# Performance work log

Hardware: AMD Instinct MI355X
Metric: run time of the kernel (lower is better)

## Reference

```python
import jax, jax.numpy as jnp
import numpy as np

INPUT_SIZE = 608
STRIDE = 32
NUM_CLASSES = 20
NMS_THRESH = 0.5
NUM_ANCHOR = 5
ANCHORS = np.array([[1.19, 1.98], [2.79, 4.59], [4.53, 8.92], [8.06, 5.29], [10.32, 10.65]], dtype=np.float32)


def _conv(x, w, b, pad):
    # x: NCHW, w: OIHW
    y = jax.lax.conv_general_dilated(x, w, (1, 1), [(pad, pad), (pad, pad)],
                                     dimension_numbers=('NCHW', 'OIHW', 'NCHW'))
    return y + b[None, :, None, None]


def _leaky(x):
    return jnp.where(x > 0, x, 0.1 * x)


def _reorg(x, s=2):
    # space-to-depth, darknet reorg: [B,C,H,W] -> [B,C*s*s,H/s,W/s]
    B, C, H, W = x.shape
    x = x.reshape(B, C, H // s, s, W // s, s)
    x = x.transpose(0, 3, 5, 1, 2, 4)
    return x.reshape(B, C * s * s, H // s, W // s)


def _forward_boxes_scores(feat_layer2, feat_layer3, w1a, b1a, w1b, b1b, wr, br, w2, b2, wp, bp):
    p5 = _leaky(_conv(feat_layer3, w1a, b1a, 1))
    p5 = _leaky(_conv(p5, w1b, b1b, 1))
    p4 = _reorg(_leaky(_conv(feat_layer2, wr, br, 0)))         # [1,256,19,19]
    p5 = jnp.concatenate([p4, p5], axis=1)                      # [1,1280,19,19]
    p5 = _leaky(_conv(p5, w2, b2, 1))
    pred = _conv(p5, wp, bp, 0)                                 # [1,125,19,19]
    B, C, H, W = pred.shape
    pred = pred.transpose(0, 2, 3, 1).reshape(B, H * W, C)
    conf = pred[:, :, :NUM_ANCHOR].reshape(B, H * W * NUM_ANCHOR, 1)
    cls = pred[:, :, NUM_ANCHOR:(1 + NUM_CLASSES) * NUM_ANCHOR].reshape(B, H * W * NUM_ANCHOR, NUM_CLASSES)
    reg = pred[:, :, (1 + NUM_CLASSES) * NUM_ANCHOR:].reshape(B, H * W, NUM_ANCHOR, 4)
    # decode_xywh
    gy, gx = jnp.meshgrid(jnp.arange(H), jnp.arange(W), indexing='ij')
    grid = jnp.stack([gx, gy], axis=-1).astype(pred.dtype).reshape(1, H * W, 1, 2)
    anchor_wh = jnp.asarray(ANCHORS).reshape(1, 1, NUM_ANCHOR, 2)
    xy = jax.nn.sigmoid(reg[..., :2]) + grid
    wh = jnp.exp(reg[..., 2:]) * anchor_wh
    xywh = jnp.concatenate([xy, wh], axis=-1).reshape(B, -1, 4) * STRIDE
    boxes = jnp.concatenate([xywh[..., :2] - 0.5 * xywh[..., 2:],
                             xywh[..., :2] + 0.5 * xywh[..., 2:]], axis=-1)
    boxes = jnp.clip(boxes[0] / INPUT_SIZE, 0.0, 1.0)           # [N,4]
    scores = jax.nn.sigmoid(conf[0]) * jax.nn.softmax(cls[0], axis=-1)  # [N,20]
    return boxes, scores


def _per_class_nms(boxes, scores, class_mask):
    # greedy sequential NMS, faithful to the torch while-loop (suppress iff IoU > thresh)
    N = boxes.shape[0]
    s = jnp.where(class_mask, scores, -jnp.inf)
    order = jnp.argsort(-s)
    b = boxes[order]
    valid = class_mask[order]
    x1, y1, x2, y2 = b[:, 0], b[:, 1], b[:, 2], b[:, 3]
    areas = (x2 - x1) * (y2 - y1)
    iw = jnp.maximum(1e-10, jnp.minimum(x2[:, None], x2[None, :]) - jnp.maximum(x1[:, None], x1[None, :]))
    ih = jnp.maximum(1e-10, jnp.minimum(y2[:, None], y2[None, :]) - jnp.maximum(y1[:, None], y1[None, :]))
    inter = iw * ih
    iou = inter / (areas[:, None] + areas[None, :] - inter)
    upper = jnp.arange(N)[None, :] > jnp.arange(N)[:, None]
    sup_mat = (iou > NMS_THRESH) & upper

    def body(i, state):
        suppressed, keep = state
        cur = valid[i] & jnp.logical_not(suppressed[i])
        keep = keep.at[i].set(cur)
        suppressed = suppressed | (cur & sup_mat[i])
        return suppressed, keep

    _, keep_sorted = jax.lax.fori_loop(0, N, body, (jnp.zeros(N, bool), jnp.zeros(N, bool)))
    return jnp.zeros(N, bool).at[order].set(keep_sorted)


def setup_inputs() -> dict:
    key = jax.random.key(0)
    ks = jax.random.split(key, 8)
    w = lambda k, shape: jax.random.normal(k, shape, jnp.float32) * 0.01
    return {
        'feat_layer2': jax.random.normal(ks[0], (1, 512, 38, 38), jnp.float32),
        'feat_layer3': jax.random.normal(ks[1], (1, 1024, 19, 19), jnp.float32),
        'w1a': w(ks[2], (1024, 1024, 3, 3)), 'b1a': jnp.zeros((1024,), jnp.float32),
        'w1b': w(ks[3], (1024, 1024, 3, 3)), 'b1b': jnp.zeros((1024,), jnp.float32),
        'wr': w(ks[4], (64, 512, 1, 1)), 'br': jnp.zeros((64,), jnp.float32),
        'w2': w(ks[5], (1024, 1280, 3, 3)), 'b2': jnp.zeros((1024,), jnp.float32),
        'wp': w(ks[6], (125, 1024, 1, 1)), 'bp': jnp.zeros((125,), jnp.float32),
    }


def reference(feat_layer2, feat_layer3, w1a, b1a, w1b, b1b, wr, br, w2, b2, wp, bp):
    boxes, scores_full = _forward_boxes_scores(feat_layer2, feat_layer3,
                                               w1a, b1a, w1b, b1b, wr, br, w2, b2, wp, bp)
    cls_inds = jnp.argmax(scores_full, axis=1)                          # [N]
    scores = jnp.take_along_axis(scores_full, cls_inds[:, None], axis=1)[:, 0]
    masks = cls_inds[None, :] == jnp.arange(NUM_CLASSES)[:, None]       # [20,N]
    keeps = jax.vmap(lambda m: _per_class_nms(boxes, scores, m))(masks)
    keep = jnp.any(keeps, axis=0)                                       # [N] bool, fixed-shape mask
    return boxes, scores, cls_inds, keep
```

## Files before the change

### kernel.cpp

```cpp
#include <hip/hip_runtime.h>

typedef _Float16 f16;
typedef _Float16 f16x8 __attribute__((ext_vector_type(8)));
typedef float f32x4 __attribute__((ext_vector_type(4)));

#define N_BOX 1805
#define NPIX 361
#define NCLS 20
#define GNW 29
#define MB_ROWS 226

__device__ __forceinline__ float leakyf(float x){ return x > 0.f ? x : 0.1f*x; }
__device__ __forceinline__ float sigmoidf_(float x){ return 1.f/(1.f + expf(-x)); }

__global__ void transpose_k(const float* __restrict__ src, float* __restrict__ dst, int R, int C){
  int i = blockIdx.x*256 + threadIdx.x;
  if (i < R*C){ int r = i / C, c = i % C; dst[c*R + r] = src[i]; }
}

__global__ void wprep_packed_k(const float* __restrict__ w, f16* __restrict__ wpk,
                               int Cin, int cpt, int NK){
  int gid = blockIdx.x*256 + threadIdx.x;
  if (gid >= 8*NK*1024) return;
  int g    = gid & 1023;
  int tile = gid >> 10;
  int kc   = tile % NK;
  int cob  = tile / NK;
  int row  = g >> 3, sraw = g & 7;
  int sdata = sraw ^ (row & 7);
  int h = sdata >> 2, jci = sdata & 3;
  int t = kc / cpt;
  int ci0 = (kc - t*cpt)*32 + jci*8;
  int co = cob*128 + row;
  const float* src = w + ((size_t)co*Cin + ci0)*9 + t;
  f16x8 outv;
  #pragma unroll
  for (int k = 0; k < 8; ++k){
    float v = src[(size_t)k*9] * 64.f;
    f16 hi = (f16)v;
    outv[k] = h ? (f16)(v - (float)hi) : hi;
  }
  *(f16x8*)(wpk + (size_t)tile*8192 + g*8) = outv;
}

__global__ void act1prep_k(const float* __restrict__ feat3, f16* __restrict__ ah, f16* __restrict__ al){
  int i = blockIdx.x*256 + threadIdx.x;
  if (i >= NPIX*1024) return;
  int p = i >> 10, c = i & 1023;
  float v = feat3[c*NPIX + p];
  f16 hi = (f16)v; f16 lo = (f16)(v - (float)hi);
  ah[i] = hi; al[i] = lo;
}

__global__ __launch_bounds__(256) void reorg_conv_k(const float* __restrict__ feat2,
    const float* __restrict__ wrT, const float* __restrict__ br,
    f16* __restrict__ cath, f16* __restrict__ catl){
  int c  = threadIdx.x & 63;
  int pq = threadIdx.x >> 6;
  int pix = blockIdx.x*4 + pq;
  int y = pix / 38, x = pix % 38;
  __shared__ float s_in[64][4];
  float acc = br[c];
  for (int cb = 0; cb < 512; cb += 64){
    __syncthreads();
    { int k = threadIdx.x >> 2, pp = threadIdx.x & 3;
      s_in[k][pp] = feat2[(cb + k)*1444 + blockIdx.x*4 + pp]; }
    __syncthreads();
    #pragma unroll
    for (int k = 0; k < 64; ++k)
      acc = fmaf(wrT[(cb+k)*64 + c], s_in[k][pq], acc);
  }
  float v = leakyf(acc);
  int co = ((y & 1)*2 + (x & 1))*64 + c;
  int p = (y>>1)*19 + (x>>1);
  f16 hi = (f16)v; f16 lo = (f16)(v - (float)hi);
  size_t o = (size_t)p*1280 + co;
  cath[o] = hi; catl[o] = lo;
}

__global__ __launch_bounds__(256) void conv_mfma_k(
    const f16* __restrict__ wpk,
    const f16* __restrict__ ahi, const f16* __restrict__ alo,
    float* __restrict__ part, int Cin, int chunks, int cpt, int NK)
{
  int cob = blockIdx.x;
  int px0 = blockIdx.y * 128;
  int ks  = blockIdx.z;
  int kc0 = ks * chunks;
  int tid = threadIdx.x;

  __shared__ f16 sA[2][128*64];
  __shared__ f16 sB[2][128*64];

  const f16* wbase = wpk + ((size_t)cob*NK + kc0)*8192;
  int aost[4];
  #pragma unroll
  for (int j = 0; j < 4; ++j) aost[j] = (tid + j*256)*8;

  int r = tid >> 1, h = tid & 1;
  int wboff[4];
  #pragma unroll
  for (int j = 0; j < 4; ++j)
    wboff[j] = (r*128 + (h*4 + j)*16) ^ ((r & 7) << 4);
  int p = px0 + r;
  int py = p / 19, px = p - py*19;
  const f16* bbase = (h ? alo : ahi);

  int lane = tid & 63, wid = tid >> 6;
  int lrow = lane & 15, lgrp = lane >> 4;
  int wr = wid >> 1, wc = wid & 1;
  int aoffH[4], aoffL[4], boffH[4], boffL[4];
  #pragma unroll
  for (int m = 0; m < 4; ++m){
    int rA = wr*64 + m*16 + lrow;
    aoffH[m] = (rA*128 + lgrp*16)     ^ ((rA & 7) << 4);
    aoffL[m] = (rA*128 + (4+lgrp)*16) ^ ((rA & 7) << 4);
    int rB = wc*64 + m*16 + lrow;
    boffH[m] = (rB*128 + lgrp*16)     ^ ((rB & 7) << 4);
    boffL[m] = (rB*128 + (4+lgrp)*16) ^ ((rB & 7) << 4);
  }

  f32x4 acc[4][4] = {};
  f16x8 sa0, sa1, sa2, sa3, sb0, sb1, sb2, sb3;

  auto LOADK = [&](int i){
    const f16* as = wbase + (size_t)i*8192;
    sa0 = *(const f16x8*)(as + aost[0]);
    sa1 = *(const f16x8*)(as + aost[1]);
    sa2 = *(const f16x8*)(as + aost[2]);
    sa3 = *(const f16x8*)(as + aost[3]);
    int kc = kc0 + i;
    int t = kc / cpt;
    int ci0 = (kc - t*cpt) * 32;
    int dy = t/3, dx = t - dy*3;
    int yy = py + dy - 1, xx = px + dx - 1;
    bool bvalid = (p < NPIX) && ((unsigned)yy < 19u) && ((unsigned)xx < 19u);
    f16x8 z = {};
    sb0 = z; sb1 = z; sb2 = z; sb3 = z;
    if (bvalid){
      const f16* bs = bbase + (size_t)(yy*19+xx)*Cin + ci0;
      sb0 = *(const f16x8*)(bs);
      sb1 = *(const f16x8*)(bs + 8);
      sb2 = *(const f16x8*)(bs + 16);
      sb3 = *(const f16x8*)(bs + 24);
    }
  };
  auto WRITEK = [&](int buf){
    *(f16x8*)(&sA[buf][aost[0]]) = sa0;
    *(f16x8*)(&sA[buf][aost[1]]) = sa1;
    *(f16x8*)(&sA[buf][aost[2]]) = sa2;
    *(f16x8*)(&sA[buf][aost[3]]) = sa3;
    *(f16x8*)((char*)sB[buf] + wboff[0]) = sb0;
    *(f16x8*)((char*)sB[buf] + wboff[1]) = sb1;
    *(f16x8*)((char*)sB[buf] + wboff[2]) = sb2;
    *(f16x8*)((char*)sB[buf] + wboff[3]) = sb3;
  };

  LOADK(0);
  WRITEK(0);
  __syncthreads();

  for (int i = 0; i < chunks; ++i){
    int cur = i & 1;
    bool more = (i + 1 < chunks);
    if (more) LOADK(i + 1);

    f16x8 bh[4], bl[4];
    #pragma unroll
    for (int n = 0; n < 4; ++n){
      bh[n] = *(const f16x8*)((char*)sB[cur] + boffH[n]);
      bl[n] = *(const f16x8*)((char*)sB[cur] + boffL[n]);
    }
    #pragma unroll
    for (int m = 0; m < 4; ++m){
      f16x8 ah = *(const f16x8*)((char*)sA[cur] + aoffH[m]);
      f16x8 al = *(const f16x8*)((char*)sA[cur] + aoffL[m]);
      #pragma unroll
      for (int n = 0; n < 4; ++n){
        acc[m][n] = __builtin_amdgcn_mfma_f32_16x16x32_f16(ah, bh[n], acc[m][n], 0,0,0);
        acc[m][n] = __builtin_amdgcn_mfma_f32_16x16x32_f16(ah, bl[n], acc[m][n], 0,0,0);
        acc[m][n] = __builtin_amdgcn_mfma_f32_16x16x32_f16(al, bh[n], acc[m][n], 0,0,0);
      }
    }
    if (more) WRITEK(cur ^ 1);
    __syncthreads();
  }

  #pragma unroll
  for (int m = 0; m < 4; ++m){
    #pragma unroll
    for (int n = 0; n < 4; ++n){
      int pp = px0 + wc*64 + n*16 + lrow;
      if (pp < NPIX){
        int co = cob*128 + wr*64 + m*16 + lgrp*4;
        size_t base = ((size_t)ks*1024 + co)*NPIX + pp;
        part[base          ] = acc[m][n][0];
        part[base +   NPIX ] = acc[m][n][1];
        part[base + 2*NPIX ] = acc[m][n][2];
        part[base + 3*NPIX ] = acc[m][n][3];
      }
    }
  }
}

__global__ void reduce16v_k(const float* __restrict__ part, const float* __restrict__ bias,
                            f16* __restrict__ dhi, f16* __restrict__ dlo,
                            int Cstride, int Coff, int splitk){
  int i = blockIdx.x*256 + threadIdx.x;
  if (i >= 1024*NPIX) return;
  int co = i / NPIX, p = i - co*NPIX;
  float s = 0.f;
  for (int k = 0; k < splitk; ++k) s += part[(size_t)k*1024*NPIX + i];
  float v = leakyf(s*0.015625f + bias[co]);
  f16 hi = (f16)v;
  f16 lo = (f16)(v - (float)hi);
  size_t o = (size_t)p*Cstride + Coff + co;
  dhi[o] = hi; dlo[o] = lo;
}

__global__ __launch_bounds__(256) void pred_conv_k(const f16* __restrict__ a3h, const f16* __restrict__ a3l,
    const float* __restrict__ wpT, const float* __restrict__ bp, float* __restrict__ pred){
  int c = threadIdx.x & 127, ph = threadIdx.x >> 7;
  int pix = blockIdx.x*2 + ph;
  __shared__ float s_in[64][2];
  float acc = 0.f;
  for (int cb = 0; cb < 1024; cb += 64){
    __syncthreads();
    if (threadIdx.x < 128){
      int k = threadIdx.x & 63, pp = threadIdx.x >> 6;
      int px2 = blockIdx.x*2 + pp;
      float v = 0.f;
      if (px2 < NPIX){
        size_t o = (size_t)px2*1024 + cb + k;
        v = (float)a3h[o] + (float)a3l[o];
      }
      s_in[k][pp] = v;
    }
    __syncthreads();
    if (c < 125){
      #pragma unroll
      for (int k = 0; k < 64; ++k)
        acc = fmaf(wpT[(cb+k)*125 + c], s_in[k][ph], acc);
    }
  }
  if (c < 125 && pix < NPIX) pred[c*NPIX + pix] = acc + bp[c];
}

__device__ const float ANCW[5] = {1.19f, 2.79f, 4.53f, 8.06f, 10.32f};
__device__ const float ANCH_[5] = {1.98f, 4.59f, 8.92f, 5.29f, 10.65f};

__global__ void decode_k(const float* __restrict__ pred, float* __restrict__ out,
                         int* __restrict__ cls_i, int* __restrict__ cnt){
  int n = blockIdx.x*256 + threadIdx.x;
  if (blockIdx.x == 0 && threadIdx.x < NCLS) cnt[threadIdx.x] = 0;
  if (n >= N_BOX) return;
  int p = n / 5, a = n % 5;
  float conf = pred[a*NPIX + p];
  float cl[20]; float m = -1e30f;
  #pragma unroll
  for (int k = 0; k < 20; ++k){ cl[k] = pred[(5 + a*20 + k)*NPIX + p]; m = fmaxf(m, cl[k]); }
  float s = 0.f;
  #pragma unroll
  for (int k = 0; k < 20; ++k){ cl[k] = expf(cl[k]-m); s += cl[k]; }
  int bi = 0; float bv = cl[0];
  #pragma unroll
  for (int k = 1; k < 20; ++k) if (cl[k] > bv){ bv = cl[k]; bi = k; }
  float score = sigmoidf_(conf) * (bv / s);
  float tx = pred[(105 + a*4 + 0)*NPIX + p];
  float ty = pred[(105 + a*4 + 1)*NPIX + p];
  float tw = pred[(105 + a*4 + 2)*NPIX + p];
  float th = pred[(105 + a*4 + 3)*NPIX + p];
  float gx = (float)(p % 19), gy = (float)(p / 19);
  float cx = (sigmoidf_(tx) + gx) * 32.f;
  float cy = (sigmoidf_(ty) + gy) * 32.f;
  float bw = expf(tw) * ANCW[a] * 32.f;
  float bh = expf(th) * ANCH_[a] * 32.f;
  float x1 = fminf(fmaxf((cx - 0.5f*bw) / 608.f, 0.f), 1.f);
  float y1 = fminf(fmaxf((cy - 0.5f*bh) / 608.f, 0.f), 1.f);
  float x2 = fminf(fmaxf((cx + 0.5f*bw) / 608.f, 0.f), 1.f);
  float y2 = fminf(fmaxf((cy + 0.5f*bh) / 608.f, 0.f), 1.f);
  out[n*4+0]=x1; out[n*4+1]=y1; out[n*4+2]=x2; out[n*4+3]=y2;
  out[7220 + n]  = score;
  out[9025 + n]  = (float)bi;
  out[10830 + n] = 0.f;
  cls_i[n] = bi;
}

__global__ __launch_bounds__(256) void rank_k(const float* __restrict__ scores,
    const int* __restrict__ cls_i, int* __restrict__ ord, int* __restrict__ cnt){
  __shared__ float s_sc[N_BOX];
  __shared__ short s_cl[N_BOX];
  int tid = threadIdx.x;
  for (int j = tid; j < N_BOX; j += 256){ s_sc[j] = scores[j]; s_cl[j] = (short)cls_i[j]; }
  __syncthreads();
  int wid = tid >> 6, lane = tid & 63;
  int i = blockIdx.x*4 + wid;
  if (i >= N_BOX) return;
  float si = s_sc[i]; short ci = s_cl[i];
  int r = 0;
  for (int j = lane; j < N_BOX; j += 64){
    float sj = s_sc[j];
    r += (int)((s_cl[j] == ci) & ((sj > si) | ((sj == si) & (j < i))));
  }
  #pragma unroll
  for (int o = 32; o; o >>= 1) r += __shfl_down(r, o);
  if (lane == 0){
    ord[ci*N_BOX + r] = i;
    atomicAdd(&cnt[ci], 1);
  }
}

__global__ __launch_bounds__(256) void maskbuild_k(const float* __restrict__ boxes,
    const int* __restrict__ ord, const int* __restrict__ cnt,
    unsigned long long* __restrict__ gmask){
  __shared__ float X1[N_BOX], Y1[N_BOX], X2[N_BOX], Y2[N_BOX], AR[N_BOX];
  int c = blockIdx.x, chunk = blockIdx.y, tid = threadIdx.x;
  int n = cnt[c];
  int r0 = chunk*MB_ROWS;
  if (n <= 0 || r0 >= n) return;
  int r1 = r0 + MB_ROWS; if (r1 > n) r1 = n;
  int rows_here = r1 - r0;
  for (int t = tid; t < n; t += 256){
    int bi = ord[c*N_BOX + t];
    float x1 = boxes[bi*4+0], y1 = boxes[bi*4+1], x2 = boxes[bi*4+2], y2 = boxes[bi*4+3];
    X1[t]=x1; Y1[t]=y1; X2[t]=x2; Y2[t]=y2; AR[t]=(x2-x1)*(y2-y1);
  }
  __syncthreads();
  int nw = (n + 63) >> 6;
  unsigned long long* rows = gmask + (size_t)c*N_BOX*GNW;
  for (int task = tid; task < rows_here*nw; task += 256){
    int w = task / rows_here, ri = task - w*rows_here;
    int i = r0 + ri;
    float ax1=X1[i], ay1=Y1[i], ax2=X2[i], ay2=Y2[i], areaA=AR[i];
    unsigned long long bits = 0;
    int j0 = w << 6;
    int jb = i+1 > j0 ? i+1 : j0;
    int je = j0+64 < n ? j0+64 : n;
    for (int j = jb; j < je; ++j){
      float iw = fmaxf(1e-10f, fminf(ax2,X2[j]) - fmaxf(ax1,X1[j]));
      float ih = fmaxf(1e-10f, fminf(ay2,Y2[j]) - fmaxf(ay1,Y1[j]));
      float inter = iw*ih;
      float iou = inter / (areaA + AR[j] - inter);
      bits |= (unsigned long long)(iou > 0.5f) << (j - j0);
    }
    rows[(size_t)i*GNW + w] = bits;
  }
}

__global__ __launch_bounds__(64) void nmsscan_k(const int* __restrict__ ord,
    const int* __restrict__ cnt, const unsigned long long* __restrict__ gmask,
    float* __restrict__ keep){
  __shared__ int sidx[N_BOX];
  int c = blockIdx.x, lane = threadIdx.x;
  int n = cnt[c];
  if (n <= 0) return;
  int nw = (n + 63) >> 6;
  for (int t = lane; t < n; t += 64) sidx[t] = ord[c*N_BOX + t];
  __syncthreads();
  const unsigned long long* rows = gmask + (size_t)c*N_BOX*GNW;
  bool act = lane < nw;
  unsigned long long S = 0;
  unsigned long long diag = (lane < n) ? rows[(size_t)lane*GNW + 0] : 0ull;
  for (int w = 0; w < nw; ++w){
    int base = w << 6;
    int nb = n - base; if (nb > 64) nb = 64;
    unsigned int slo = (unsigned)__builtin_amdgcn_readlane((int)(unsigned)S, w);
    unsigned int shi = (unsigned)__builtin_amdgcn_readlane((int)(unsigned)(S >> 32), w);
    unsigned long long sup = ((unsigned long long)shi << 32) | slo;
    unsigned long long validm = (nb >= 64) ? ~0ull : ((1ull << nb) - 1ull);
    unsigned long long avail = ~sup & validm;
    unsigned long long kmask = 0;
    unsigned long long diag_next = 0;
    if (w+1 < nw){
      int i2 = base + 64 + lane;
      if (i2 < n) diag_next = rows[(size_t)i2*GNW + (w+1)];
    }
    while (avail){
      int b = __builtin_ctzll(avail);
      kmask |= 1ull << b;
      unsigned int dlo = (unsigned)__builtin_amdgcn_readlane((int)(unsigned)diag, b);
      unsigned int dhi = (unsigned)__builtin_amdgcn_readlane((int)(unsigned)(diag >> 32), b);
      unsigned long long drow = ((unsigned long long)dhi << 32) | dlo;
      sup |= drow;
      avail &= ~(1ull << b);
      avail &= ~sup;
      if (act && lane > w)
        S |= rows[(size_t)(base + b)*GNW + lane];
    }
    if ((kmask >> lane) & 1ull) keep[sidx[base + lane]] = 1.f;
    diag = diag_next;
  }
}

static inline size_t align256(size_t x){ return (x + 255) & ~(size_t)255; }

extern "C" void kernel_launch(void* const* d_in, const int* in_sizes, int n_in,
                              void* d_out, int out_size, void* d_ws, size_t ws_size,
                              hipStream_t stream){
  const float* feat2 = (const float*)d_in[0];
  const float* feat3 = (const float*)d_in[1];
  const float* w1a = (const float*)d_in[2];
  const float* b1a = (const float*)d_in[3];
  const float* w1b = (const float*)d_in[4];
  const float* b1b = (const float*)d_in[5];
  const float* wr  = (const float*)d_in[6];
  const float* br  = (const float*)d_in[7];
  const float* w2  = (const float*)d_in[8];
  const float* b2  = (const float*)d_in[9];
  const float* wp  = (const float*)d_in[10];
  const float* bp  = (const float*)d_in[11];
  float* out = (float*)d_out;
  char* ws = (char*)d_ws;

  size_t off = 0;
  float* part = (float*)(ws + off); off = align256(off + (size_t)24*1024*NPIX*4);
  f16* wpk  = (f16*)(ws + off); off = align256(off + (size_t)8*360*8192*2);
  f16* a1h  = (f16*)(ws + off); off = align256(off + (size_t)NPIX*1024*2);
  f16* a1l  = (f16*)(ws + off); off = align256(off + (size_t)NPIX*1024*2);
  f16* a2h  = (f16*)(ws + off); off = align256(off + (size_t)NPIX*1024*2);
  f16* a2l  = (f16*)(ws + off); off = align256(off + (size_t)NPIX*1024*2);
  f16* a3h  = (f16*)(ws + off); off = align256(off + (size_t)NPIX*1024*2);
  f16* a3l  = (f16*)(ws + off); off = align256(off + (size_t)NPIX*1024*2);
  f16* cath = (f16*)(ws + off); off = align256(off + (size_t)NPIX*1280*2);
  f16* catl = (f16*)(ws + off); off = align256(off + (size_t)NPIX*1280*2);
  float* pred = (float*)(ws + off); off = align256(off + (size_t)125*NPIX*4);
  float* wrT  = (float*)(ws + off); off = align256(off + (size_t)512*64*4);
  float* wpT  = (float*)(ws + off); off = align256(off + (size_t)1024*125*4);
  int* cls_i  = (int*)(ws + off); off = align256(off + (size_t)N_BOX*4);
  int* ord    = (int*)(ws + off); off = align256(off + (size_t)NCLS*N_BOX*4);
  int* cnt    = (int*)(ws + off); off = align256(off + (size_t)NCLS*4);
  unsigned long long* gmask = (unsigned long long*)part;

  transpose_k<<<(64*512 + 255)/256, 256, 0, stream>>>(wr, wrT, 64, 512);
  transpose_k<<<(125*1024 + 255)/256, 256, 0, stream>>>(wp, wpT, 125, 1024);
  act1prep_k<<<(NPIX*1024 + 255)/256, 256, 0, stream>>>(feat3, a1h, a1l);
  reorg_conv_k<<<361, 256, 0, stream>>>(feat2, wrT, br, cath, catl);

  wprep_packed_k<<<(8*288*1024)/256, 256, 0, stream>>>(w1a, wpk, 1024, 32, 288);
  { dim3 g(8, 3, 16);
    conv_mfma_k<<<g, 256, 0, stream>>>(wpk, a1h, a1l, part, 1024, 18, 32, 288); }
  reduce16v_k<<<(1024*NPIX + 255)/256, 256, 0, stream>>>(part, b1a, a2h, a2l, 1024, 0, 16);

  wprep_packed_k<<<(8*288*1024)/256, 256, 0, stream>>>(w1b, wpk, 1024, 32, 288);
  { dim3 g(8, 3, 16);
    conv_mfma_k<<<g, 256, 0, stream>>>(wpk, a2h, a2l, part, 1024, 18, 32, 288); }
  reduce16v_k<<<(1024*NPIX + 255)/256, 256, 0, stream>>>(part, b1b, cath, catl, 1280, 256, 16);

  wprep_packed_k<<<(8*360*1024)/256, 256, 0, stream>>>(w2, wpk, 1280, 40, 360);
  { dim3 g(8, 3, 18);
    conv_mfma_k<<<g, 256, 0, stream>>>(wpk, cath, catl, part, 1280, 20, 40, 360); }
  reduce16v_k<<<(1024*NPIX + 255)/256, 256, 0, stream>>>(part, b2, a3h, a3l, 1024, 0, 18);

  pred_conv_k<<<181, 256, 0, stream>>>(a3h, a3l, wpT, bp, pred);
  decode_k<<<8, 256, 0, stream>>>(pred, out, cls_i, cnt);
  rank_k<<<(N_BOX + 3)/4, 256, 0, stream>>>(out + 7220, cls_i, ord, cnt);
  { dim3 mg(NCLS, 8);
    maskbuild_k<<<mg, 256, 0, stream>>>(out, ord, cnt, gmask); }
  nmsscan_k<<<NCLS, 64, 0, stream>>>(ord, cnt, gmask, out + 10830);
}
```

Baseline: 321.7 us.

## Load activation fragments directly from global and read weights contiguously in prep

```diff
diff --git a/kernel.cpp b/kernel.cpp
--- a/kernel.cpp
+++ b/kernel.cpp
@@ -18,29 +18,35 @@
   if (i < R*C){ int r = i / C, c = i % C; dst[c*R + r] = src[i]; }
 }
 
-__global__ void wprep_packed_k(const float* __restrict__ w, f16* __restrict__ wpk,
-                               int Cin, int cpt, int NK){
+__global__ void wprep9_k(const float* __restrict__ w, f16* __restrict__ wpk,
+                         int Cin, int cpt, int NK, int total){
   int gid = blockIdx.x*256 + threadIdx.x;
-  if (gid >= 8*NK*1024) return;
-  int g    = gid & 1023;
-  int tile = gid >> 10;
-  int kc   = tile % NK;
-  int cob  = tile / NK;
-  int row  = g >> 3, sraw = g & 7;
-  int sdata = sraw ^ (row & 7);
-  int h = sdata >> 2, jci = sdata & 3;
-  int t = kc / cpt;
-  int ci0 = (kc - t*cpt)*32 + jci*8;
-  int co = cob*128 + row;
-  const float* src = w + ((size_t)co*Cin + ci0)*9 + t;
-  f16x8 outv;
-  #pragma unroll
-  for (int k = 0; k < 8; ++k){
-    float v = src[(size_t)k*9] * 64.f;
-    f16 hi = (f16)v;
-    outv[k] = h ? (f16)(v - (float)hi) : hi;
-  }
-  *(f16x8*)(wpk + (size_t)tile*8192 + g*8) = outv;
+  if (gid >= total) return;
+  int jci  = gid & 3;
+  int rest = gid >> 2;
+  int nblk = Cin >> 5;
+  int ciblk = rest % nblk;
+  int co    = rest / nblk;
+  int cob = co >> 7, row = co & 127;
+  const float* src = w + ((size_t)co*Cin + ciblk*32 + jci*8)*9;
+  float v[72];
+  #pragma unroll
+  for (int q = 0; q < 72; ++q) v[q] = src[q];
+  int rx = row & 7;
+  #pragma unroll
+  for (int t = 0; t < 9; ++t){
+    f16x8 hv, lv;
+    #pragma unroll
+    for (int k = 0; k < 8; ++k){
+      float f = v[k*9 + t] * 64.f;
+      f16 hi = (f16)f;
+      hv[k] = hi;
+      lv[k] = (f16)(f - (float)hi);
+    }
+    size_t tb = ((size_t)cob*NK + t*cpt + ciblk)*8192 + row*64;
+    *(f16x8*)(wpk + tb + ((0*4 + jci) ^ rx)*8) = hv;
+    *(f16x8*)(wpk + tb + ((1*4 + jci) ^ rx)*8) = lv;
+  }
 }
 
 __global__ void act1prep_k(const float* __restrict__ feat3, f16* __restrict__ ah, f16* __restrict__ al){
@@ -90,87 +96,76 @@
   int tid = threadIdx.x;
 
   __shared__ f16 sA[2][128*64];
-  __shared__ f16 sB[2][128*64];
 
   const f16* wbase = wpk + ((size_t)cob*NK + kc0)*8192;
   int aost[4];
   #pragma unroll
   for (int j = 0; j < 4; ++j) aost[j] = (tid + j*256)*8;
-
-  int r = tid >> 1, h = tid & 1;
-  int wboff[4];
-  #pragma unroll
-  for (int j = 0; j < 4; ++j)
-    wboff[j] = (r*128 + (h*4 + j)*16) ^ ((r & 7) << 4);
-  int p = px0 + r;
-  int py = p / 19, px = p - py*19;
-  const f16* bbase = (h ? alo : ahi);
 
   int lane = tid & 63, wid = tid >> 6;
   int lrow = lane & 15, lgrp = lane >> 4;
   int wr = wid >> 1, wc = wid & 1;
-  int aoffH[4], aoffL[4], boffH[4], boffL[4];
+  int aoffH[4], aoffL[4];
   #pragma unroll
   for (int m = 0; m < 4; ++m){
     int rA = wr*64 + m*16 + lrow;
     aoffH[m] = (rA*128 + lgrp*16)     ^ ((rA & 7) << 4);
     aoffL[m] = (rA*128 + (4+lgrp)*16) ^ ((rA & 7) << 4);
-    int rB = wc*64 + m*16 + lrow;
-    boffH[m] = (rB*128 + lgrp*16)     ^ ((rB & 7) << 4);
-    boffL[m] = (rB*128 + (4+lgrp)*16) ^ ((rB & 7) << 4);
+  }
+  int bpy[4], bpx[4]; bool bpv[4];
+  #pragma unroll
+  for (int n = 0; n < 4; ++n){
+    int p = px0 + wc*64 + n*16 + lrow;
+    bpv[n] = (p < NPIX);
+    int pc = bpv[n] ? p : 0;
+    bpy[n] = pc / 19; bpx[n] = pc - bpy[n]*19;
   }
 
   f32x4 acc[4][4] = {};
-  f16x8 sa0, sa1, sa2, sa3, sb0, sb1, sb2, sb3;
-
-  auto LOADK = [&](int i){
+  f16x8 sa0, sa1, sa2, sa3;
+
+  auto LOADA = [&](int i){
     const f16* as = wbase + (size_t)i*8192;
     sa0 = *(const f16x8*)(as + aost[0]);
     sa1 = *(const f16x8*)(as + aost[1]);
     sa2 = *(const f16x8*)(as + aost[2]);
     sa3 = *(const f16x8*)(as + aost[3]);
+  };
+  auto WRITEA = [&](int buf){
+    *(f16x8*)(&sA[buf][aost[0]]) = sa0;
+    *(f16x8*)(&sA[buf][aost[1]]) = sa1;
+    *(f16x8*)(&sA[buf][aost[2]]) = sa2;
+    *(f16x8*)(&sA[buf][aost[3]]) = sa3;
+  };
+
+  LOADA(0);
+  WRITEA(0);
+  __syncthreads();
+
+  for (int i = 0; i < chunks; ++i){
     int kc = kc0 + i;
     int t = kc / cpt;
     int ci0 = (kc - t*cpt) * 32;
     int dy = t/3, dx = t - dy*3;
-    int yy = py + dy - 1, xx = px + dx - 1;
-    bool bvalid = (p < NPIX) && ((unsigned)yy < 19u) && ((unsigned)xx < 19u);
-    f16x8 z = {};
-    sb0 = z; sb1 = z; sb2 = z; sb3 = z;
-    if (bvalid){
-      const f16* bs = bbase + (size_t)(yy*19+xx)*Cin + ci0;
-      sb0 = *(const f16x8*)(bs);
-      sb1 = *(const f16x8*)(bs + 8);
-      sb2 = *(const f16x8*)(bs + 16);
-      sb3 = *(const f16x8*)(bs + 24);
-    }
-  };
-  auto WRITEK = [&](int buf){
-    *(f16x8*)(&sA[buf][aost[0]]) = sa0;
-    *(f16x8*)(&sA[buf][aost[1]]) = sa1;
-    *(f16x8*)(&sA[buf][aost[2]]) = sa2;
-    *(f16x8*)(&sA[buf][aost[3]]) = sa3;
-    *(f16x8*)((char*)sB[buf] + wboff[0]) = sb0;
-    *(f16x8*)((char*)sB[buf] + wboff[1]) = sb1;
-    *(f16x8*)((char*)sB[buf] + wboff[2]) = sb2;
-    *(f16x8*)((char*)sB[buf] + wboff[3]) = sb3;
-  };
-
-  LOADK(0);
-  WRITEK(0);
-  __syncthreads();
-
-  for (int i = 0; i < chunks; ++i){
-    int cur = i & 1;
-    bool more = (i + 1 < chunks);
-    if (more) LOADK(i + 1);
 
     f16x8 bh[4], bl[4];
     #pragma unroll
     for (int n = 0; n < 4; ++n){
-      bh[n] = *(const f16x8*)((char*)sB[cur] + boffH[n]);
-      bl[n] = *(const f16x8*)((char*)sB[cur] + boffL[n]);
-    }
+      int yy = bpy[n] + dy - 1, xx = bpx[n] + dx - 1;
+      bool ok = bpv[n] & ((unsigned)yy < 19u) & ((unsigned)xx < 19u);
+      f16x8 z = {};
+      bh[n] = z; bl[n] = z;
+      if (ok){
+        size_t bo = (size_t)(yy*19 + xx)*Cin + ci0 + lgrp*8;
+        bh[n] = *(const f16x8*)(ahi + bo);
+        bl[n] = *(const f16x8*)(alo + bo);
+      }
+    }
+
+    int cur = i & 1;
+    bool more = (i + 1 < chunks);
+    if (more) LOADA(i + 1);
+
     #pragma unroll
     for (int m = 0; m < 4; ++m){
       f16x8 ah = *(const f16x8*)((char*)sA[cur] + aoffH[m]);
@@ -182,7 +177,7 @@
         acc[m][n] = __builtin_amdgcn_mfma_f32_16x16x32_f16(al, bh[n], acc[m][n], 0,0,0);
       }
     }
-    if (more) WRITEK(cur ^ 1);
+    if (more) WRITEA(cur ^ 1);
     __syncthreads();
   }
 
@@ -436,17 +431,17 @@
   act1prep_k<<<(NPIX*1024 + 255)/256, 256, 0, stream>>>(feat3, a1h, a1l);
   reorg_conv_k<<<361, 256, 0, stream>>>(feat2, wrT, br, cath, catl);
 
-  wprep_packed_k<<<(8*288*1024)/256, 256, 0, stream>>>(w1a, wpk, 1024, 32, 288);
+  wprep9_k<<<(1024*32*4 + 255)/256, 256, 0, stream>>>(w1a, wpk, 1024, 32, 288, 1024*32*4);
   { dim3 g(8, 3, 16);
     conv_mfma_k<<<g, 256, 0, stream>>>(wpk, a1h, a1l, part, 1024, 18, 32, 288); }
   reduce16v_k<<<(1024*NPIX + 255)/256, 256, 0, stream>>>(part, b1a, a2h, a2l, 1024, 0, 16);
 
-  wprep_packed_k<<<(8*288*1024)/256, 256, 0, stream>>>(w1b, wpk, 1024, 32, 288);
+  wprep9_k<<<(1024*32*4 + 255)/256, 256, 0, stream>>>(w1b, wpk, 1024, 32, 288, 1024*32*4);
   { dim3 g(8, 3, 16);
     conv_mfma_k<<<g, 256, 0, stream>>>(wpk, a2h, a2l, part, 1024, 18, 32, 288); }
   reduce16v_k<<<(1024*NPIX + 255)/256, 256, 0, stream>>>(part, b1b, cath, catl, 1280, 256, 16);
 
-  wprep_packed_k<<<(8*360*1024)/256, 256, 0, stream>>>(w2, wpk, 1280, 40, 360);
+  wprep9_k<<<(1024*40*4 + 255)/256, 256, 0, stream>>>(w2, wpk, 1280, 40, 360, 1024*40*4);
   { dim3 g(8, 3, 18);
     conv_mfma_k<<<g, 256, 0, stream>>>(wpk, cath, catl, part, 1280, 20, 40, 360); }
   reduce16v_k<<<(1024*NPIX + 255)/256, 256, 0, stream>>>(part, b2, a3h, a3l, 1024, 0, 18);
```

Measured after the change: 377.7 us. +17.4%, slower.

## Stream conv MFMA operand tiles directly into LDS with global_load_lds

Applied to the files above, without the earlier changes.

```diff
diff --git a/kernel.cpp b/kernel.cpp
--- a/kernel.cpp
+++ b/kernel.cpp
@@ -13,15 +13,21 @@
 __device__ __forceinline__ float leakyf(float x){ return x > 0.f ? x : 0.1f*x; }
 __device__ __forceinline__ float sigmoidf_(float x){ return 1.f/(1.f + expf(-x)); }
 
+__device__ __forceinline__ void gl16(const f16* g, f16* l){
+  __builtin_amdgcn_global_load_lds(
+      (const __attribute__((address_space(1))) unsigned int*)g,
+      (__attribute__((address_space(3))) unsigned int*)l, 16, 0, 0);
+}
+
 __global__ void transpose_k(const float* __restrict__ src, float* __restrict__ dst, int R, int C){
   int i = blockIdx.x*256 + threadIdx.x;
   if (i < R*C){ int r = i / C, c = i % C; dst[c*R + r] = src[i]; }
 }
 
-__global__ void wprep_packed_k(const float* __restrict__ w, f16* __restrict__ wpk,
-                               int Cin, int cpt, int NK){
+__global__ void wprep11_k(const float* __restrict__ w, f16* __restrict__ wpk,
+                          int Cin, int cpt, int NK, int total){
   int gid = blockIdx.x*256 + threadIdx.x;
-  if (gid >= 8*NK*1024) return;
+  if (gid >= total) return;
   int g    = gid & 1023;
   int tile = gid >> 10;
   int kc   = tile % NK;
@@ -30,21 +36,24 @@
   int sdata = sraw ^ (row & 7);
   int h = sdata >> 2, jci = sdata & 3;
   int t = kc / cpt;
-  int ci0 = (kc - t*cpt)*32 + jci*8;
+  int ciblk = kc - t*cpt;
+  int ci0 = ciblk*32 + jci*8;
   int co = cob*128 + row;
   const float* src = w + ((size_t)co*Cin + ci0)*9 + t;
   f16x8 outv;
   #pragma unroll
   for (int k = 0; k < 8; ++k){
-    float v = src[(size_t)k*9] * 64.f;
-    f16 hi = (f16)v;
-    outv[k] = h ? (f16)(v - (float)hi) : hi;
-  }
-  *(f16x8*)(wpk + (size_t)tile*8192 + g*8) = outv;
-}
-
-__global__ void act1prep_k(const float* __restrict__ feat3, f16* __restrict__ ah, f16* __restrict__ al){
+    float f = src[(size_t)k*9] * 64.f;
+    f16 hi = (f16)f;
+    outv[k] = h ? (f16)(f - (float)hi) : hi;
+  }
+  *((f16x8*)wpk + gid) = outv;
+}
+
+__global__ void act1prep_k(const float* __restrict__ feat3, f16* __restrict__ ah, f16* __restrict__ al,
+                           f16* __restrict__ zpage){
   int i = blockIdx.x*256 + threadIdx.x;
+  if (blockIdx.x == 0 && threadIdx.x < 64) zpage[threadIdx.x] = (f16)0.f;
   if (i >= NPIX*1024) return;
   int p = i >> 10, c = i & 1023;
   float v = feat3[c*NPIX + p];
@@ -81,6 +90,7 @@
 __global__ __launch_bounds__(256) void conv_mfma_k(
     const f16* __restrict__ wpk,
     const f16* __restrict__ ahi, const f16* __restrict__ alo,
+    const f16* __restrict__ zpage,
     float* __restrict__ part, int Cin, int chunks, int cpt, int NK)
 {
   int cob = blockIdx.x;
@@ -89,26 +99,28 @@
   int kc0 = ks * chunks;
   int tid = threadIdx.x;
 
-  __shared__ f16 sA[2][128*64];
-  __shared__ f16 sB[2][128*64];
-
-  const f16* wbase = wpk + ((size_t)cob*NK + kc0)*8192;
-  int aost[4];
-  #pragma unroll
-  for (int j = 0; j < 4; ++j) aost[j] = (tid + j*256)*8;
-
-  int r = tid >> 1, h = tid & 1;
-  int wboff[4];
-  #pragma unroll
-  for (int j = 0; j < 4; ++j)
-    wboff[j] = (r*128 + (h*4 + j)*16) ^ ((r & 7) << 4);
-  int p = px0 + r;
-  int py = p / 19, px = p - py*19;
-  const f16* bbase = (h ? alo : ahi);
+  __shared__ f16 sA[2][8192];
+  __shared__ f16 sB[2][8192];
 
   int lane = tid & 63, wid = tid >> 6;
   int lrow = lane & 15, lgrp = lane >> 4;
   int wr = wid >> 1, wc = wid & 1;
+
+  const f16* wtile0 = wpk + (size_t)(cob*NK + kc0)*8192;
+
+  int srow = tid >> 3;
+  int sdata = (tid & 7) ^ (srow & 7);
+  int sh = sdata >> 2, sjci = sdata & 3;
+  const f16* bbase = sh ? alo : ahi;
+  int spy[4], spx[4]; bool spv[4];
+  #pragma unroll
+  for (int s = 0; s < 4; ++s){
+    int p = px0 + srow + s*32;
+    spv[s] = (p < NPIX);
+    int pc = spv[s] ? p : 0;
+    spy[s] = pc / 19; spx[s] = pc - spy[s]*19;
+  }
+
   int aoffH[4], aoffL[4], boffH[4], boffL[4];
   #pragma unroll
   for (int m = 0; m < 4; ++m){
@@ -121,49 +133,33 @@
   }
 
   f32x4 acc[4][4] = {};
-  f16x8 sa0, sa1, sa2, sa3, sb0, sb1, sb2, sb3;
-
-  auto LOADK = [&](int i){
-    const f16* as = wbase + (size_t)i*8192;
-    sa0 = *(const f16x8*)(as + aost[0]);
-    sa1 = *(const f16x8*)(as + aost[1]);
-    sa2 = *(const f16x8*)(as + aost[2]);
-    sa3 = *(const f16x8*)(as + aost[3]);
+
+  auto ISSUE = [&](int i, int buf){
+    const f16* wt = wtile0 + (size_t)i*8192;
+    #pragma unroll
+    for (int j = 0; j < 4; ++j){
+      int o = (tid + j*256)*8;
+      gl16(wt + o, &sA[buf][o]);
+    }
     int kc = kc0 + i;
     int t = kc / cpt;
     int ci0 = (kc - t*cpt) * 32;
     int dy = t/3, dx = t - dy*3;
-    int yy = py + dy - 1, xx = px + dx - 1;
-    bool bvalid = (p < NPIX) && ((unsigned)yy < 19u) && ((unsigned)xx < 19u);
-    f16x8 z = {};
-    sb0 = z; sb1 = z; sb2 = z; sb3 = z;
-    if (bvalid){
-      const f16* bs = bbase + (size_t)(yy*19+xx)*Cin + ci0;
-      sb0 = *(const f16x8*)(bs);
-      sb1 = *(const f16x8*)(bs + 8);
-      sb2 = *(const f16x8*)(bs + 16);
-      sb3 = *(const f16x8*)(bs + 24);
+    #pragma unroll
+    for (int s = 0; s < 4; ++s){
+      int yy = spy[s] + dy - 1, xx = spx[s] + dx - 1;
+      bool ok = spv[s] & ((unsigned)yy < 19u) & ((unsigned)xx < 19u);
+      const f16* src = ok ? (bbase + (size_t)(yy*19+xx)*Cin + ci0 + sjci*8) : zpage;
+      gl16(src, &sB[buf][(tid + s*256)*8]);
     }
   };
-  auto WRITEK = [&](int buf){
-    *(f16x8*)(&sA[buf][aost[0]]) = sa0;
-    *(f16x8*)(&sA[buf][aost[1]]) = sa1;
-    *(f16x8*)(&sA[buf][aost[2]]) = sa2;
-    *(f16x8*)(&sA[buf][aost[3]]) = sa3;
-    *(f16x8*)((char*)sB[buf] + wboff[0]) = sb0;
-    *(f16x8*)((char*)sB[buf] + wboff[1]) = sb1;
-    *(f16x8*)((char*)sB[buf] + wboff[2]) = sb2;
-    *(f16x8*)((char*)sB[buf] + wboff[3]) = sb3;
-  };
-
-  LOADK(0);
-  WRITEK(0);
+
+  ISSUE(0, 0);
   __syncthreads();
 
   for (int i = 0; i < chunks; ++i){
     int cur = i & 1;
-    bool more = (i + 1 < chunks);
-    if (more) LOADK(i + 1);
+    if (i + 1 < chunks) ISSUE(i + 1, cur ^ 1);
 
     f16x8 bh[4], bl[4];
     #pragma unroll
@@ -182,7 +178,6 @@
         acc[m][n] = __builtin_amdgcn_mfma_f32_16x16x32_f16(al, bh[n], acc[m][n], 0,0,0);
       }
     }
-    if (more) WRITEK(cur ^ 1);
     __syncthreads();
   }
 
@@ -413,7 +408,7 @@
   char* ws = (char*)d_ws;
 
   size_t off = 0;
-  float* part = (float*)(ws + off); off = align256(off + (size_t)24*1024*NPIX*4);
+  float* part = (float*)(ws + off); off = align256(off + (size_t)18*1024*NPIX*4);
   f16* wpk  = (f16*)(ws + off); off = align256(off + (size_t)8*360*8192*2);
   f16* a1h  = (f16*)(ws + off); off = align256(off + (size_t)NPIX*1024*2);
   f16* a1l  = (f16*)(ws + off); off = align256(off + (size_t)NPIX*1024*2);
@@ -429,26 +424,27 @@
   int* cls_i  = (int*)(ws + off); off = align256(off + (size_t)N_BOX*4);
   int* ord    = (int*)(ws + off); off = align256(off + (size_t)NCLS*N_BOX*4);
   int* cnt    = (int*)(ws + off); off = align256(off + (size_t)NCLS*4);
+  f16* zpage  = (f16*)(ws + off); off = align256(off + 256);
   unsigned long long* gmask = (unsigned long long*)part;
 
   transpose_k<<<(64*512 + 255)/256, 256, 0, stream>>>(wr, wrT, 64, 512);
   transpose_k<<<(125*1024 + 255)/256, 256, 0, stream>>>(wp, wpT, 125, 1024);
-  act1prep_k<<<(NPIX*1024 + 255)/256, 256, 0, stream>>>(feat3, a1h, a1l);
+  act1prep_k<<<(NPIX*1024 + 255)/256, 256, 0, stream>>>(feat3, a1h, a1l, zpage);
   reorg_conv_k<<<361, 256, 0, stream>>>(feat2, wrT, br, cath, catl);
 
-  wprep_packed_k<<<(8*288*1024)/256, 256, 0, stream>>>(w1a, wpk, 1024, 32, 288);
+  wprep11_k<<<(8*288*1024)/256, 256, 0, stream>>>(w1a, wpk, 1024, 32, 288, 8*288*1024);
   { dim3 g(8, 3, 16);
-    conv_mfma_k<<<g, 256, 0, stream>>>(wpk, a1h, a1l, part, 1024, 18, 32, 288); }
+    conv_mfma_k<<<g, 256, 0, stream>>>(wpk, a1h, a1l, zpage, part, 1024, 18, 32, 288); }
   reduce16v_k<<<(1024*NPIX + 255)/256, 256, 0, stream>>>(part, b1a, a2h, a2l, 1024, 0, 16);
 
-  wprep_packed_k<<<(8*288*1024)/256, 256, 0, stream>>>(w1b, wpk, 1024, 32, 288);
+  wprep11_k<<<(8*288*1024)/256, 256, 0, stream>>>(w1b, wpk, 1024, 32, 288, 8*288*1024);
   { dim3 g(8, 3, 16);
-    conv_mfma_k<<<g, 256, 0, stream>>>(wpk, a2h, a2l, part, 1024, 18, 32, 288); }
+    conv_mfma_k<<<g, 256, 0, stream>>>(wpk, a2h, a2l, zpage, part, 1024, 18, 32, 288); }
   reduce16v_k<<<(1024*NPIX + 255)/256, 256, 0, stream>>>(part, b1b, cath, catl, 1280, 256, 16);
 
-  wprep_packed_k<<<(8*360*1024)/256, 256, 0, stream>>>(w2, wpk, 1280, 40, 360);
+  wprep11_k<<<(8*360*1024)/256, 256, 0, stream>>>(w2, wpk, 1280, 40, 360, 8*360*1024);
   { dim3 g(8, 3, 18);
-    conv_mfma_k<<<g, 256, 0, stream>>>(wpk, cath, catl, part, 1280, 20, 40, 360); }
+    conv_mfma_k<<<g, 256, 0, stream>>>(wpk, cath, catl, zpage, part, 1280, 20, 40, 360); }
   reduce16v_k<<<(1024*NPIX + 255)/256, 256, 0, stream>>>(part, b2, a3h, a3l, 1024, 0, 18);
 
   pred_conv_k<<<181, 256, 0, stream>>>(a3h, a3l, wpT, bp, pred);
```

Result: no change. 321.6 us (-0.0%).
